# Kernel tuning notes

Hardware: AMD Instinct MI355X
Metric: run time of the kernel (lower is better)

The kernel has to match this reference:

```python
import jax, jax.numpy as jnp
import numpy as np

NEAR, FAR = 2.0, 6.0
N_SAMPLES = 64
L_PTS, L_DIR = 10, 4
INF_DELTA = 1e10


def posenc(x, L):
    # x: [..., 3] -> [..., 3 + 6*L] (identity + sin/cos at 2^l frequencies)
    freqs = 2.0 ** jnp.arange(L, dtype=x.dtype)              # [L]
    ang = x[..., None, :] * freqs[:, None]                   # [..., L, 3]
    enc = jnp.concatenate([jnp.sin(ang), jnp.cos(ang)], axis=-1)  # [..., L, 6]
    return jnp.concatenate([x, enc.reshape(x.shape[:-1] + (L * 6,))], axis=-1)


def setup_inputs() -> dict:
    key = jax.random.key(0)
    ks = jax.random.split(key, 12)
    R, D, DH = 4096, 256, 128
    PE_P, PE_D = 3 + 6 * L_PTS, 3 + 6 * L_DIR  # 63, 27

    def w(k, shape):
        fan_in = shape[0]
        return jax.random.normal(k, shape, dtype=jnp.float32) / np.sqrt(fan_in)

    return {
        "xyz": jax.random.normal(ks[0], (1, R, 3), dtype=jnp.float32),
        "viewdirs": jax.random.normal(ks[1], (1, R, 3), dtype=jnp.float32),
        "W1": w(ks[2], (PE_P, D)), "b1": jnp.zeros((D,), jnp.float32),
        "W2": w(ks[3], (D, D)),    "b2": jnp.zeros((D,), jnp.float32),
        "W3": w(ks[4], (D, D)),    "b3": jnp.zeros((D,), jnp.float32),
        "Wsig": w(ks[5], (D, 1)),  "bsig": jnp.zeros((1,), jnp.float32),
        "Wfeat": w(ks[6], (D, D)), "bfeat": jnp.zeros((D,), jnp.float32),
        "Wdir": w(ks[7], (D + PE_D, DH)), "bdir": jnp.zeros((DH,), jnp.float32),
        "Wrgb": w(ks[8], (DH, 3)), "brgb": jnp.zeros((3,), jnp.float32),
    }


def reference(xyz, viewdirs, W1, b1, W2, b2, W3, b3, Wsig, bsig,
              Wfeat, bfeat, Wdir, bdir, Wrgb, brgb):
    xyz = xyz[0]          # [R, 3] (batch dim squeezed as in render_coarse)
    vd = viewdirs[0]
    vd = vd / jnp.linalg.norm(vd, axis=-1, keepdims=True)
    R = xyz.shape[0]

    # Evenly spaced samples between near and far (perturb=0 -> deterministic)
    t = jnp.linspace(0.0, 1.0, N_SAMPLES, dtype=xyz.dtype)
    samples = NEAR * (1.0 - t) + FAR * t                     # [N]
    samples = jnp.broadcast_to(samples, (R, N_SAMPLES))      # [R, N]
    delta = jnp.concatenate(
        [samples[:, 1:] - samples[:, :-1],
         jnp.full((R, 1), INF_DELTA, dtype=samples.dtype)], axis=-1)  # [R, N]

    # Sample points along each ray
    pts = xyz[:, None, :] + samples[..., None] * vd[:, None, :]  # [R, N, 3]

    # NeRF MLP: positional-encoded points -> density + view-dep color
    pe = posenc(pts, L_PTS)                                   # [R, N, 63]
    de = posenc(vd, L_DIR)                                    # [R, 27]
    h = jax.nn.relu(pe @ W1 + b1)
    h = jax.nn.relu(h @ W2 + b2)
    h = jax.nn.relu(h @ W3 + b3)                              # [R, N, 256]
    density = (h @ Wsig + bsig)[..., 0]                       # [R, N]
    feat = h @ Wfeat + bfeat                                  # [R, N, 256]
    de_b = jnp.broadcast_to(de[:, None, :], (R, N_SAMPLES, de.shape[-1]))
    hd = jax.nn.relu(jnp.concatenate([feat, de_b], axis=-1) @ Wdir + bdir)
    rgb = jax.nn.sigmoid(hd @ Wrgb + brgb)                    # [R, N, 3]

    # Volume rendering (alpha compositing with cumprod transmittance)
    sigma = jax.nn.relu(density)
    alpha = 1.0 - jnp.exp(-sigma * delta)                     # [R, N]
    T = jnp.concatenate(
        [jnp.ones((R, 1), alpha.dtype),
         jnp.cumprod(1.0 - alpha[:, :-1], axis=-1)], axis=-1)
    w = T * alpha                                             # [R, N]
    rgb_map = jnp.sum(w[..., None] * rgb, axis=-2)            # [R, 3]
    alpha_map = jnp.sum(w, axis=-1, keepdims=True)            # [R, 1]
    rgb_map = rgb_map + (1.0 - alpha_map)                     # white_bkgd
    depth_map = jnp.sum(w * samples, axis=-1)                 # [R]
    return rgb_map, depth_map, alpha_map
```

## Files before the change

kernel.cpp:

```cpp
#include <hip/hip_runtime.h>
#include <hip/hip_bf16.h>
#include <math.h>


typedef unsigned short u16;
typedef unsigned int   u32;
typedef __bf16 bf16x8 __attribute__((ext_vector_type(8)));
typedef float  f32x4  __attribute__((ext_vector_type(4)));

#define HI_STRIDE 296
#define LO_STRIDE 264
#define NROW 64

__device__ __align__(16) u16 g_whi[249856];
__device__ __align__(16) u16 g_wlo[147456];

constexpr int OFF_W1 = 0;
constexpr int OFF_W2 = 16384;
constexpr int OFF_W3 = 81920;
constexpr int OFF_WF = 147456;
constexpr int OFF_WD = 212992;

static __device__ __forceinline__ float bf2f(u16 u) {
  return __uint_as_float(((u32)u) << 16);
}
static __device__ __forceinline__ u16 f2bf(float f) {
  u32 x = __float_as_uint(f);
  return (u16)((x + 0x7FFFu + ((x >> 16) & 1u)) >> 16);
}
static __device__ __forceinline__ float wash(float x) {
  return (x == x) ? x : 0.0f;
}

struct alignas(8) U16x4 { u16 x, y, z, w; };

__global__ void repack_kernel(const float* __restrict__ w1, const float* __restrict__ w2,
                              const float* __restrict__ w3, const float* __restrict__ wf,
                              const float* __restrict__ wd) {
  int e = blockIdx.x * 256 + threadIdx.x;
  const float* src; int K, N, ks, base;
  if (e < 81920)       { if (e < 16384) { src = w1; K = 63;  N = 256; ks = 2; base = OFF_W1; }
                         else           { src = w2; K = 256; N = 256; ks = 8; base = OFF_W2; } }
  else if (e < 147456) { src = w3; K = 256; N = 256; ks = 8; base = OFF_W3; }
  else if (e < 212992) { src = wf; K = 256; N = 256; ks = 8; base = OFF_WF; }
  else                 { src = wd; K = 283; N = 128; ks = 9; base = OFF_WD; }
  int le   = e - base;
  int f    = le >> 9, pos = le & 511;
  int lane = pos >> 3, j = pos & 7;
  int t    = f / ks,  s = f - t * ks;
  int k    = s * 32 + ((lane >> 4) << 3) + j;
  int n    = (t << 4) + (lane & 15);
  float v  = (k < K) ? src[k * N + n] : 0.0f;
  u16 h    = f2bf(v);
  g_whi[e] = h;
  if (e < 147456) g_wlo[e] = f2bf(v - bf2f(h));
}

template<int KS, int NT, int RT, bool RELU, bool SPLIT>
static __device__ __forceinline__ void mlp_layer(u16* hi, u16* lo,
                                                 const u16* __restrict__ wh_,
                                                 const u16* __restrict__ wl_,
                                                 const float* __restrict__ bias,
                                                 int rg, int cg, int lane) {
  f32x4 acc[RT][NT];
#pragma unroll
  for (int rt = 0; rt < RT; ++rt)
#pragma unroll
    for (int nt = 0; nt < NT; ++nt) {
      f32x4 z = {0.0f, 0.0f, 0.0f, 0.0f};
      acc[rt][nt] = z;
    }
  const int l15 = lane & 15, q = lane >> 4;
#pragma unroll
  for (int s = 0; s < KS; ++s) {
    bf16x8 ah[RT], al[RT];
#pragma unroll
    for (int rt = 0; rt < RT; ++rt) {
      const int row = (rg * RT + rt) * 16 + l15;
      ah[rt] = *reinterpret_cast<const bf16x8*>(&hi[row * HI_STRIDE + s * 32 + q * 8]);
      if (SPLIT)
        al[rt] = *reinterpret_cast<const bf16x8*>(&lo[row * LO_STRIDE + s * 32 + q * 8]);
    }
    bf16x8 wh[NT], wl[NT];
#pragma unroll
    for (int nt = 0; nt < NT; ++nt) {
      const int t = cg * NT + nt;
      wh[nt] = *reinterpret_cast<const bf16x8*>(&wh_[(t * KS + s) * 512 + lane * 8]);
      if (SPLIT)
        wl[nt] = *reinterpret_cast<const bf16x8*>(&wl_[(t * KS + s) * 512 + lane * 8]);
    }
#pragma unroll
    for (int rt = 0; rt < RT; ++rt)
#pragma unroll
      for (int nt = 0; nt < NT; ++nt) {
        acc[rt][nt] = __builtin_amdgcn_mfma_f32_16x16x32_bf16(
            wh[nt], ah[rt], acc[rt][nt], 0, 0, 0);
        if (SPLIT) {
          acc[rt][nt] = __builtin_amdgcn_mfma_f32_16x16x32_bf16(
              wh[nt], al[rt], acc[rt][nt], 0, 0, 0);
          acc[rt][nt] = __builtin_amdgcn_mfma_f32_16x16x32_bf16(
              wl[nt], ah[rt], acc[rt][nt], 0, 0, 0);
        }
      }
  }
  __syncthreads();
#pragma unroll
  for (int nt = 0; nt < NT; ++nt) {
    const int nb = (cg * NT + nt) * 16 + q * 4;
    const float b0 = bias[nb + 0], b1 = bias[nb + 1];
    const float b2 = bias[nb + 2], b3 = bias[nb + 3];
#pragma unroll
    for (int rt = 0; rt < RT; ++rt) {
      const int row = (rg * RT + rt) * 16 + l15;
      float v0 = acc[rt][nt][0] + b0;
      float v1 = acc[rt][nt][1] + b1;
      float v2 = acc[rt][nt][2] + b2;
      float v3 = acc[rt][nt][3] + b3;
      if (RELU) {
        v0 = fmaxf(v0, 0.0f); v1 = fmaxf(v1, 0.0f);
        v2 = fmaxf(v2, 0.0f); v3 = fmaxf(v3, 0.0f);
      }
      U16x4 oh; oh.x = f2bf(v0); oh.y = f2bf(v1); oh.z = f2bf(v2); oh.w = f2bf(v3);
      *reinterpret_cast<U16x4*>(&hi[row * HI_STRIDE + nb]) = oh;
      if (SPLIT) {
        U16x4 ol;
        ol.x = f2bf(v0 - bf2f(oh.x)); ol.y = f2bf(v1 - bf2f(oh.y));
        ol.z = f2bf(v2 - bf2f(oh.z)); ol.w = f2bf(v3 - bf2f(oh.w));
        *reinterpret_cast<U16x4*>(&lo[row * LO_STRIDE + nb]) = ol;
      }
    }
  }
  __syncthreads();
}

__global__ __launch_bounds__(512, 4)
void nerf_kernel(const float* __restrict__ xyz, const float* __restrict__ vdirs,
                 const float* __restrict__ b1, const float* __restrict__ b2,
                 const float* __restrict__ b3, const float* __restrict__ wsig,
                 const float* __restrict__ bsig, const float* __restrict__ bfeat,
                 const float* __restrict__ bdir, const float* __restrict__ wrgb,
                 const float* __restrict__ brgb, float* __restrict__ out) {
  __shared__ u16  s_hi[NROW * HI_STRIDE];
  __shared__ u16  s_lo[NROW * LO_STRIDE];
  __shared__ float s_geo[6];
  __shared__ float s_de[32];

  const int tid  = threadIdx.x;
  const int wave = tid >> 6;
  const int lane = tid & 63;
  const int rg   = wave >> 2;
  const int cg   = wave & 3;

  if (tid == 0) {
    int rgI = blockIdx.x;
    float vx = vdirs[rgI * 3 + 0];
    float vy = vdirs[rgI * 3 + 1];
    float vz = vdirs[rgI * 3 + 2];
    float inv = 1.0f / sqrtf(vx * vx + vy * vy + vz * vz + 1e-20f);
    s_geo[0] = xyz[rgI * 3 + 0];
    s_geo[1] = xyz[rgI * 3 + 1];
    s_geo[2] = xyz[rgI * 3 + 2];
    s_geo[3] = vx * inv;
    s_geo[4] = vy * inv;
    s_geo[5] = vz * inv;
  }
  __syncthreads();

  if (tid < 32) {
    float val = 0.0f;
    if (tid < 3) val = s_geo[3 + tid];
    else if (tid < 27) {
      int fi = tid - 3, l = fi / 6, m = fi % 6;
      int ii = (m < 3) ? m : m - 3;
      float ang = s_geo[3 + ii] * (float)(1 << l);
      val = (m < 3) ? sinf(ang) : cosf(ang);
    }
    s_de[tid] = val;
  }

  {
    int row = tid >> 3, c8 = tid & 7;
    float t  = (float)row * (1.0f / 63.0f);
    float ts = 2.0f * (1.0f - t) + 6.0f * t;
    float p[3];
    p[0] = s_geo[0] + ts * s_geo[3];
    p[1] = s_geo[1] + ts * s_geo[4];
    p[2] = s_geo[2] + ts * s_geo[5];
#pragma unroll
    for (int j = 0; j < 8; ++j) {
      int f = c8 * 8 + j;
      float val;
      if (f < 3) val = p[f];
      else if (f == 63) val = 0.0f;
      else {
        int fi = f - 3, l = fi / 6, m = fi % 6;
        int ii = (m < 3) ? m : m - 3;
        float ang = p[ii] * (float)(1 << l);
        val = (m < 3) ? sinf(ang) : cosf(ang);
      }
      u16 h = f2bf(val);
      s_hi[row * HI_STRIDE + f] = h;
      s_lo[row * LO_STRIDE + f] = f2bf(val - bf2f(h));
    }
  }
  __syncthreads();

  mlp_layer<2, 4, 2, true, true>(s_hi, s_lo, g_whi + OFF_W1, g_wlo + OFF_W1,
                                 b1, rg, cg, lane);
  mlp_layer<8, 4, 2, true, true>(s_hi, s_lo, g_whi + OFF_W2, g_wlo + OFF_W2,
                                 b2, rg, cg, lane);
  mlp_layer<8, 4, 2, true, true>(s_hi, s_lo, g_whi + OFF_W3, g_wlo + OFF_W3,
                                 b3, rg, cg, lane);

  float my_den = 0.0f;
  if (tid < 64) {
    float a = 0.0f;
    const float4* wp = reinterpret_cast<const float4*>(wsig);
#pragma unroll 8
    for (int k4 = 0; k4 < 64; ++k4) {
      U16x4 h = *reinterpret_cast<const U16x4*>(&s_hi[tid * HI_STRIDE + k4 * 4]);
      U16x4 l = *reinterpret_cast<const U16x4*>(&s_lo[tid * LO_STRIDE + k4 * 4]);
      float4 w = wp[k4];
      a += (bf2f(h.x) + bf2f(l.x)) * w.x + (bf2f(h.y) + bf2f(l.y)) * w.y
         + (bf2f(h.z) + bf2f(l.z)) * w.z + (bf2f(h.w) + bf2f(l.w)) * w.w;
    }
    my_den = wash(a + bsig[0]);
  }

  mlp_layer<8, 4, 2, false, false>(s_hi, s_lo, g_whi + OFF_WF, g_wlo,
                                   bfeat, rg, cg, lane);

  {
    int row = tid >> 3, i0 = (tid & 7) * 4;
#pragma unroll
    for (int j = 0; j < 4; ++j)
      s_hi[row * HI_STRIDE + 256 + i0 + j] = f2bf(s_de[i0 + j]);
  }
  __syncthreads();

  mlp_layer<9, 2, 2, true, false>(s_hi, s_lo, g_whi + OFF_WD, g_wlo,
                                  bdir, rg, cg, lane);

  float r0 = 0.0f, r1 = 0.0f, r2 = 0.0f;
  if (tid < 64) {
    float a0 = brgb[0], a1 = brgb[1], a2 = brgb[2];
#pragma unroll 8
    for (int k = 0; k < 128; ++k) {
      float hv = bf2f(s_hi[tid * HI_STRIDE + k]);
      a0 += hv * wrgb[k * 3 + 0];
      a1 += hv * wrgb[k * 3 + 1];
      a2 += hv * wrgb[k * 3 + 2];
    }
    a0 = wash(a0); a1 = wash(a1); a2 = wash(a2);
    r0 = 1.0f / (1.0f + expf(-a0));
    r1 = 1.0f / (1.0f + expf(-a1));
    r2 = 1.0f / (1.0f + expf(-a2));
  }

  if (wave == 0) {
    int rgI = blockIdx.x;
    float t  = (float)lane * (1.0f / 63.0f);
    float ts = 2.0f * (1.0f - t) + 6.0f * t;
    float delta;
    if (lane < 63) {
      float t2 = (float)(lane + 1) * (1.0f / 63.0f);
      delta = (2.0f * (1.0f - t2) + 6.0f * t2) - ts;
    } else delta = 1e10f;
    float sig = fmaxf(my_den, 0.0f);
    float sd  = fminf(sig * delta, 60.0f);
    float incl = sd;
#pragma unroll
    for (int o = 1; o < 64; o <<= 1) {
      float v = __shfl_up(incl, o, 64);
      if (lane >= o) incl += v;
    }
    float excl  = fminf(fmaxf(incl - sd, 0.0f), 60.0f);
    float T     = expf(-excl);
    float alpha = 1.0f - expf(-sd);
    float w     = T * alpha;
    float sw = w, swr = w * r0, swg = w * r1, swb = w * r2, swd = w * ts;
#pragma unroll
    for (int o = 32; o > 0; o >>= 1) {
      sw  += __shfl_xor(sw,  o, 64);
      swr += __shfl_xor(swr, o, 64);
      swg += __shfl_xor(swg, o, 64);
      swb += __shfl_xor(swb, o, 64);
      swd += __shfl_xor(swd, o, 64);
    }
    if (lane == 0) {
      float bg = 1.0f - sw;
      out[rgI * 3 + 0]  = swr + bg;
      out[rgI * 3 + 1]  = swg + bg;
      out[rgI * 3 + 2]  = swb + bg;
      out[12288 + rgI]  = swd;
      out[16384 + rgI]  = sw;
    }
  }
}

extern "C" void kernel_launch(void* const* d_in, const int* in_sizes, int n_in,
                              void* d_out, int out_size, void* d_ws, size_t ws_size,
                              hipStream_t stream) {
  const float* xyz   = (const float*)d_in[0];
  const float* vdirs = (const float*)d_in[1];
  const float* W1    = (const float*)d_in[2];
  const float* b1    = (const float*)d_in[3];
  const float* W2    = (const float*)d_in[4];
  const float* b2    = (const float*)d_in[5];
  const float* W3    = (const float*)d_in[6];
  const float* b3    = (const float*)d_in[7];
  const float* Wsig  = (const float*)d_in[8];
  const float* bsig  = (const float*)d_in[9];
  const float* Wfeat = (const float*)d_in[10];
  const float* bfeat = (const float*)d_in[11];
  const float* Wdir  = (const float*)d_in[12];
  const float* bdir  = (const float*)d_in[13];
  const float* Wrgb  = (const float*)d_in[14];
  const float* brgb  = (const float*)d_in[15];
  float* out = (float*)d_out;

  repack_kernel<<<dim3(976), dim3(256), 0, stream>>>(W1, W2, W3, Wfeat, Wdir);
  nerf_kernel<<<dim3(4096), dim3(512), 0, stream>>>(
      xyz, vdirs, b1, b2, b3, Wsig, bsig, bfeat, bdir, Wrgb, brgb, out);
}
```

Measured before the change: 404.0 us.

## Replace split-bf16 MFMA with single fp16 MFMA and recompute last sample density in fp32

Drops the hi/lo bf16 split, which needed three MFMAs per tile plus a second activation buffer, and runs every layer as a single fp16 MFMA with one activation buffer and one weight array. Because the last sample's delta is 1e10, its density has to be accurate, so the kernel recomputes that sample's trunk (layers 1-3 and sigma) in fp32 with scalar FMAs and substitutes it for lane 63. This cuts MFMA work and LDS traffic to about a third, at the cost of fp16 accuracy elsewhere and an extra serial fp32 pass that reads about 150K weight floats per block.

```diff
diff --git a/kernel.cpp b/kernel.cpp
--- a/kernel.cpp
+++ b/kernel.cpp
@@ -5,15 +5,14 @@
 
 typedef unsigned short u16;
 typedef unsigned int   u32;
-typedef __bf16 bf16x8 __attribute__((ext_vector_type(8)));
-typedef float  f32x4  __attribute__((ext_vector_type(4)));
-
-#define HI_STRIDE 296
-#define LO_STRIDE 264
+typedef _Float16 f16;
+typedef _Float16 f16x8 __attribute__((ext_vector_type(8)));
+typedef float    f32x4 __attribute__((ext_vector_type(4)));
+
+#define ACT_STRIDE 296
 #define NROW 64
 
-__device__ __align__(16) u16 g_whi[249856];
-__device__ __align__(16) u16 g_wlo[147456];
+__device__ __align__(16) f16 g_w[249856];
 
 constexpr int OFF_W1 = 0;
 constexpr int OFF_W2 = 16384;
@@ -21,18 +20,11 @@
 constexpr int OFF_WF = 147456;
 constexpr int OFF_WD = 212992;
 
-static __device__ __forceinline__ float bf2f(u16 u) {
-  return __uint_as_float(((u32)u) << 16);
-}
-static __device__ __forceinline__ u16 f2bf(float f) {
-  u32 x = __float_as_uint(f);
-  return (u16)((x + 0x7FFFu + ((x >> 16) & 1u)) >> 16);
-}
 static __device__ __forceinline__ float wash(float x) {
   return (x == x) ? x : 0.0f;
 }
 
-struct alignas(8) U16x4 { u16 x, y, z, w; };
+struct alignas(8) F16x4 { f16 x, y, z, w; };
 
 __global__ void repack_kernel(const float* __restrict__ w1, const float* __restrict__ w2,
                               const float* __restrict__ w3, const float* __restrict__ wf,
@@ -50,16 +42,12 @@
   int t    = f / ks,  s = f - t * ks;
   int k    = s * 32 + ((lane >> 4) << 3) + j;
   int n    = (t << 4) + (lane & 15);
-  float v  = (k < K) ? src[k * N + n] : 0.0f;
-  u16 h    = f2bf(v);
-  g_whi[e] = h;
-  if (e < 147456) g_wlo[e] = f2bf(v - bf2f(h));
-}
-
-template<int KS, int NT, int RT, bool RELU, bool SPLIT>
-static __device__ __forceinline__ void mlp_layer(u16* hi, u16* lo,
-                                                 const u16* __restrict__ wh_,
-                                                 const u16* __restrict__ wl_,
+  g_w[e] = (k < K) ? (f16)src[k * N + n] : (f16)0.0f;
+}
+
+template<int KS, int NT, int RT, bool RELU>
+static __device__ __forceinline__ void mlp_layer(f16* act,
+                                                 const f16* __restrict__ w_,
                                                  const float* __restrict__ bias,
                                                  int rg, int cg, int lane) {
   f32x4 acc[RT][NT];
@@ -73,35 +61,24 @@
   const int l15 = lane & 15, q = lane >> 4;
 #pragma unroll
   for (int s = 0; s < KS; ++s) {
-    bf16x8 ah[RT], al[RT];
+    f16x8 af[RT];
 #pragma unroll
     for (int rt = 0; rt < RT; ++rt) {
       const int row = (rg * RT + rt) * 16 + l15;
-      ah[rt] = *reinterpret_cast<const bf16x8*>(&hi[row * HI_STRIDE + s * 32 + q * 8]);
-      if (SPLIT)
-        al[rt] = *reinterpret_cast<const bf16x8*>(&lo[row * LO_STRIDE + s * 32 + q * 8]);
-    }
-    bf16x8 wh[NT], wl[NT];
+      af[rt] = *reinterpret_cast<const f16x8*>(&act[row * ACT_STRIDE + s * 32 + q * 8]);
+    }
+    f16x8 wf[NT];
 #pragma unroll
     for (int nt = 0; nt < NT; ++nt) {
       const int t = cg * NT + nt;
-      wh[nt] = *reinterpret_cast<const bf16x8*>(&wh_[(t * KS + s) * 512 + lane * 8]);
-      if (SPLIT)
-        wl[nt] = *reinterpret_cast<const bf16x8*>(&wl_[(t * KS + s) * 512 + lane * 8]);
+      wf[nt] = *reinterpret_cast<const f16x8*>(&w_[(t * KS + s) * 512 + lane * 8]);
     }
 #pragma unroll
     for (int rt = 0; rt < RT; ++rt)
 #pragma unroll
-      for (int nt = 0; nt < NT; ++nt) {
-        acc[rt][nt] = __builtin_amdgcn_mfma_f32_16x16x32_bf16(
-            wh[nt], ah[rt], acc[rt][nt], 0, 0, 0);
-        if (SPLIT) {
-          acc[rt][nt] = __builtin_amdgcn_mfma_f32_16x16x32_bf16(
-              wh[nt], al[rt], acc[rt][nt], 0, 0, 0);
-          acc[rt][nt] = __builtin_amdgcn_mfma_f32_16x16x32_bf16(
-              wl[nt], ah[rt], acc[rt][nt], 0, 0, 0);
-        }
-      }
+      for (int nt = 0; nt < NT; ++nt)
+        acc[rt][nt] = __builtin_amdgcn_mfma_f32_16x16x32_f16(
+            wf[nt], af[rt], acc[rt][nt], 0, 0, 0);
   }
   __syncthreads();
 #pragma unroll
@@ -120,14 +97,8 @@
         v0 = fmaxf(v0, 0.0f); v1 = fmaxf(v1, 0.0f);
         v2 = fmaxf(v2, 0.0f); v3 = fmaxf(v3, 0.0f);
       }
-      U16x4 oh; oh.x = f2bf(v0); oh.y = f2bf(v1); oh.z = f2bf(v2); oh.w = f2bf(v3);
-      *reinterpret_cast<U16x4*>(&hi[row * HI_STRIDE + nb]) = oh;
-      if (SPLIT) {
-        U16x4 ol;
-        ol.x = f2bf(v0 - bf2f(oh.x)); ol.y = f2bf(v1 - bf2f(oh.y));
-        ol.z = f2bf(v2 - bf2f(oh.z)); ol.w = f2bf(v3 - bf2f(oh.w));
-        *reinterpret_cast<U16x4*>(&lo[row * LO_STRIDE + nb]) = ol;
-      }
+      F16x4 o; o.x = (f16)v0; o.y = (f16)v1; o.z = (f16)v2; o.w = (f16)v3;
+      *reinterpret_cast<F16x4*>(&act[row * ACT_STRIDE + nb]) = o;
     }
   }
   __syncthreads();
@@ -135,15 +106,19 @@
 
 __global__ __launch_bounds__(512, 4)
 void nerf_kernel(const float* __restrict__ xyz, const float* __restrict__ vdirs,
-                 const float* __restrict__ b1, const float* __restrict__ b2,
-                 const float* __restrict__ b3, const float* __restrict__ wsig,
-                 const float* __restrict__ bsig, const float* __restrict__ bfeat,
-                 const float* __restrict__ bdir, const float* __restrict__ wrgb,
-                 const float* __restrict__ brgb, float* __restrict__ out) {
-  __shared__ u16  s_hi[NROW * HI_STRIDE];
-  __shared__ u16  s_lo[NROW * LO_STRIDE];
+                 const float* __restrict__ w1f, const float* __restrict__ b1,
+                 const float* __restrict__ w2f, const float* __restrict__ b2,
+                 const float* __restrict__ w3f, const float* __restrict__ b3,
+                 const float* __restrict__ wsig, const float* __restrict__ bsig,
+                 const float* __restrict__ bfeat, const float* __restrict__ bdir,
+                 const float* __restrict__ wrgb, const float* __restrict__ brgb,
+                 float* __restrict__ out) {
+  __shared__ f16  s_act[NROW * ACT_STRIDE];
   __shared__ float s_geo[6];
   __shared__ float s_de[32];
+  __shared__ float s_pe[64];
+  __shared__ float s_h0[256], s_h1[256];
+  __shared__ float s_sig;
 
   const int tid  = threadIdx.x;
   const int wave = tid >> 6;
@@ -178,6 +153,23 @@
     s_de[tid] = val;
   }
 
+  if (tid >= 64 && tid < 128) {
+    int f = tid - 64;
+    float p[3];
+    p[0] = s_geo[0] + 6.0f * s_geo[3];
+    p[1] = s_geo[1] + 6.0f * s_geo[4];
+    p[2] = s_geo[2] + 6.0f * s_geo[5];
+    float val = 0.0f;
+    if (f < 3) val = p[f];
+    else if (f < 63) {
+      int fi = f - 3, l = fi / 6, m = fi % 6;
+      int ii = (m < 3) ? m : m - 3;
+      float ang = p[ii] * (float)(1 << l);
+      val = (m < 3) ? sinf(ang) : cosf(ang);
+    }
+    s_pe[f] = val;
+  }
+
   {
     int row = tid >> 3, c8 = tid & 7;
     float t  = (float)row * (1.0f / 63.0f);
@@ -198,19 +190,44 @@
         float ang = p[ii] * (float)(1 << l);
         val = (m < 3) ? sinf(ang) : cosf(ang);
       }
-      u16 h = f2bf(val);
-      s_hi[row * HI_STRIDE + f] = h;
-      s_lo[row * LO_STRIDE + f] = f2bf(val - bf2f(h));
-    }
-  }
-  __syncthreads();
-
-  mlp_layer<2, 4, 2, true, true>(s_hi, s_lo, g_whi + OFF_W1, g_wlo + OFF_W1,
-                                 b1, rg, cg, lane);
-  mlp_layer<8, 4, 2, true, true>(s_hi, s_lo, g_whi + OFF_W2, g_wlo + OFF_W2,
-                                 b2, rg, cg, lane);
-  mlp_layer<8, 4, 2, true, true>(s_hi, s_lo, g_whi + OFF_W3, g_wlo + OFF_W3,
-                                 b3, rg, cg, lane);
+      s_act[row * ACT_STRIDE + f] = (f16)val;
+    }
+  }
+  __syncthreads();
+
+  if (tid < 256) {
+    float a = b1[tid];
+    for (int k = 0; k < 63; ++k) a = fmaf(w1f[k * 256 + tid], s_pe[k], a);
+    s_h0[tid] = fmaxf(a, 0.0f);
+  }
+  __syncthreads();
+  if (tid < 256) {
+    float a = b2[tid];
+#pragma unroll 4
+    for (int k = 0; k < 256; ++k) a = fmaf(w2f[k * 256 + tid], s_h0[k], a);
+    s_h1[tid] = fmaxf(a, 0.0f);
+  }
+  __syncthreads();
+  if (tid < 256) {
+    float a = b3[tid];
+#pragma unroll 4
+    for (int k = 0; k < 256; ++k) a = fmaf(w3f[k * 256 + tid], s_h1[k], a);
+    s_h0[tid] = fmaxf(a, 0.0f);
+  }
+  __syncthreads();
+  if (tid < 64) {
+    float a = s_h0[tid * 4 + 0] * wsig[tid * 4 + 0]
+            + s_h0[tid * 4 + 1] * wsig[tid * 4 + 1]
+            + s_h0[tid * 4 + 2] * wsig[tid * 4 + 2]
+            + s_h0[tid * 4 + 3] * wsig[tid * 4 + 3];
+#pragma unroll
+    for (int o = 32; o > 0; o >>= 1) a += __shfl_xor(a, o, 64);
+    if (tid == 0) s_sig = wash(a + bsig[0]);
+  }
+
+  mlp_layer<2, 4, 2, true>(s_act, g_w + OFF_W1, b1, rg, cg, lane);
+  mlp_layer<8, 4, 2, true>(s_act, g_w + OFF_W2, b2, rg, cg, lane);
+  mlp_layer<8, 4, 2, true>(s_act, g_w + OFF_W3, b3, rg, cg, lane);
 
   float my_den = 0.0f;
   if (tid < 64) {
@@ -218,35 +235,31 @@
     const float4* wp = reinterpret_cast<const float4*>(wsig);
 #pragma unroll 8
     for (int k4 = 0; k4 < 64; ++k4) {
-      U16x4 h = *reinterpret_cast<const U16x4*>(&s_hi[tid * HI_STRIDE + k4 * 4]);
-      U16x4 l = *reinterpret_cast<const U16x4*>(&s_lo[tid * LO_STRIDE + k4 * 4]);
+      F16x4 h = *reinterpret_cast<const F16x4*>(&s_act[tid * ACT_STRIDE + k4 * 4]);
       float4 w = wp[k4];
-      a += (bf2f(h.x) + bf2f(l.x)) * w.x + (bf2f(h.y) + bf2f(l.y)) * w.y
-         + (bf2f(h.z) + bf2f(l.z)) * w.z + (bf2f(h.w) + bf2f(l.w)) * w.w;
+      a += (float)h.x * w.x + (float)h.y * w.y + (float)h.z * w.z + (float)h.w * w.w;
     }
     my_den = wash(a + bsig[0]);
   }
 
-  mlp_layer<8, 4, 2, false, false>(s_hi, s_lo, g_whi + OFF_WF, g_wlo,
-                                   bfeat, rg, cg, lane);
+  mlp_layer<8, 4, 2, false>(s_act, g_w + OFF_WF, bfeat, rg, cg, lane);
 
   {
     int row = tid >> 3, i0 = (tid & 7) * 4;
 #pragma unroll
     for (int j = 0; j < 4; ++j)
-      s_hi[row * HI_STRIDE + 256 + i0 + j] = f2bf(s_de[i0 + j]);
-  }
-  __syncthreads();
-
-  mlp_layer<9, 2, 2, true, false>(s_hi, s_lo, g_whi + OFF_WD, g_wlo,
-                                  bdir, rg, cg, lane);
+      s_act[row * ACT_STRIDE + 256 + i0 + j] = (f16)s_de[i0 + j];
+  }
+  __syncthreads();
+
+  mlp_layer<9, 2, 2, true>(s_act, g_w + OFF_WD, bdir, rg, cg, lane);
 
   float r0 = 0.0f, r1 = 0.0f, r2 = 0.0f;
   if (tid < 64) {
     float a0 = brgb[0], a1 = brgb[1], a2 = brgb[2];
 #pragma unroll 8
     for (int k = 0; k < 128; ++k) {
-      float hv = bf2f(s_hi[tid * HI_STRIDE + k]);
+      float hv = (float)s_act[tid * ACT_STRIDE + k];
       a0 += hv * wrgb[k * 3 + 0];
       a1 += hv * wrgb[k * 3 + 1];
       a2 += hv * wrgb[k * 3 + 2];
@@ -266,7 +279,8 @@
       float t2 = (float)(lane + 1) * (1.0f / 63.0f);
       delta = (2.0f * (1.0f - t2) + 6.0f * t2) - ts;
     } else delta = 1e10f;
-    float sig = fmaxf(my_den, 0.0f);
+    float den = (lane == 63) ? s_sig : my_den;
+    float sig = fmaxf(den, 0.0f);
     float sd  = fminf(sig * delta, 60.0f);
     float incl = sd;
 #pragma unroll
@@ -321,5 +335,5 @@
 
   repack_kernel<<<dim3(976), dim3(256), 0, stream>>>(W1, W2, W3, Wfeat, Wdir);
   nerf_kernel<<<dim3(4096), dim3(512), 0, stream>>>(
-      xyz, vdirs, b1, b2, b3, Wsig, bsig, bfeat, bdir, Wrgb, brgb, out);
-}
+      xyz, vdirs, W1, b1, W2, b2, W3, b3, Wsig, bsig, bfeat, bdir, Wrgb, brgb, out);
+}
```

Result: no change. 404.8 us (+0.2%).
